# Optimization experiments

Hardware: AMD Instinct MI355X
Metric: run time of the kernel (lower is better)

The kernel has to match this reference:

```python
import jax, jax.numpy as jnp
import numpy as np

DIM = 256
HEADS = 8
WS = 8          # window_size[0]
N = WS * WS     # tokens per window
B = 2048        # number of windows (batch * windows_per_image)


def _rel_pos_indices(ws):
    # Reproduces: grid of (i,j) positions flattened, pairwise diff, shifted, flattened index
    pos = np.arange(ws)
    gy, gx = np.meshgrid(pos, pos, indexing='ij')
    grid = np.stack([gy.ravel(), gx.ravel()], axis=-1)          # (ws*ws, 2)
    rel = grid[:, None, :] - grid[None, :, :] + (ws - 1)        # (n, n, 2)
    idx = rel[..., 0] * (2 * ws - 1) + rel[..., 1]              # (n, n)
    return jnp.asarray(idx, dtype=jnp.int32)


def setup_inputs() -> dict:
    key = jax.random.key(0)
    ks = jax.random.split(key, 6)
    return {
        'x': jax.random.normal(ks[0], (B, N, DIM), dtype=jnp.float32),
        'qkv_w': jax.random.normal(ks[1], (3 * DIM, DIM), dtype=jnp.float32) * 0.02,
        'qkv_b': jax.random.normal(ks[2], (3 * DIM,), dtype=jnp.float32) * 0.02,
        'proj_w': jax.random.normal(ks[3], (DIM, DIM), dtype=jnp.float32) * 0.02,
        'proj_b': jax.random.normal(ks[4], (DIM,), dtype=jnp.float32) * 0.02,
        'bias_table': jax.random.normal(ks[5], ((2 * WS - 1) ** 2, HEADS), dtype=jnp.float32) * 0.02,
        'rel_pos_indices': _rel_pos_indices(WS),
    }


def reference(x, qkv_w, qkv_b, proj_w, proj_b, bias_table, rel_pos_indices):
    b, n, c = x.shape
    head_dim = c // HEADS
    scale = head_dim ** (-0.5)

    qkv = x @ qkv_w.T + qkv_b                                   # [b, n, 3c]
    q, k, v = jnp.split(qkv, 3, axis=-1)
    # b n (h d) -> b h n d
    to_heads = lambda t: t.reshape(b, n, HEADS, head_dim).transpose(0, 2, 1, 3)
    q, k, v = to_heads(q) * scale, to_heads(k), to_heads(v)

    # relative position bias: [n, n, h] -> [h, n, n]
    bias = bias_table[rel_pos_indices].transpose(2, 0, 1)

    attn = jnp.einsum('bhnd,bhmd->bhnm', q, k) + bias           # [b, h, n, n]
    attn = jax.nn.softmax(attn, axis=-1)
    out = jnp.einsum('bhnm,bhmd->bhnd', attn, v)                # [b, h, n, d]
    out = out.transpose(0, 2, 1, 3).reshape(b, n, c)
    out = out @ proj_w.T + proj_b
    return (out, attn)
```

## Files before the change

### kernel.cpp

```cpp
#include <hip/hip_runtime.h>

typedef __bf16 bf16;
typedef __attribute__((ext_vector_type(8))) __bf16 bf16x8;
typedef __attribute__((ext_vector_type(4))) __bf16 bf16x4;
typedef __attribute__((ext_vector_type(4))) float f32x4;

#define MFMA16(A, Bf, Cf) __builtin_amdgcn_mfma_f32_16x16x32_bf16((A), (Bf), (Cf), 0, 0, 0)

namespace {
constexpr int kB = 2048;
constexpr int kN = 64;
constexpr int kC = 256;
constexpr int kH = 8;
constexpr float kScale = 0.17677669529663687f;
constexpr size_t kOut0 = (size_t)kB * kN * kC;
constexpr size_t kWqkvOff = 0;
constexpr size_t kWprojOff = 393216;
constexpr size_t kBiasOff = 524288;
}

__global__ void prep_kernel(const float* __restrict__ qkv_w,
                            const float* __restrict__ proj_w,
                            const float* __restrict__ bias_table,
                            const int* __restrict__ rel_idx,
                            bf16* __restrict__ qkv_wb,
                            bf16* __restrict__ proj_wb,
                            float* __restrict__ biasf) {
  int t = blockIdx.x * 256 + threadIdx.x;
  if (t < 196608) {
    qkv_wb[t] = (bf16)qkv_w[t];
  } else if (t < 262144) {
    int u = t - 196608;
    proj_wb[u] = (bf16)proj_w[u];
  } else if (t < 294912) {
    int u = t - 262144;
    int h = u >> 12;
    int v = u & 4095;
    int wv = v >> 10;
    int ct = (v >> 8) & 3;
    int lane = (v >> 2) & 63;
    int r = v & 3;
    int row = wv * 16 + (lane >> 4) * 4 + r;
    int col = ct * 16 + (lane & 15);
    biasf[u] = bias_table[rel_idx[row * 64 + col] * 8 + h];
  }
}

__launch_bounds__(256, 3)
__global__ void attn_kernel(const float* __restrict__ x,
                            const float* __restrict__ qkv_b,
                            const float* __restrict__ proj_b,
                            const bf16* __restrict__ qkv_wb,
                            const bf16* __restrict__ proj_wb,
                            const float* __restrict__ biasf,
                            float* __restrict__ out,
                            float* __restrict__ attn_out) {
  __shared__ __align__(16) bf16 xo[64 * 264];
  __shared__ __align__(16) bf16 qp[64 * 72];
  __shared__ __align__(16) bf16 kh[64 * 40];
  __shared__ __align__(16) bf16 vT[32 * 72];

  const int t = threadIdx.x;
  const int wave = t >> 6;
  const int lane = t & 63;
  const int l16 = lane & 15;
  const int quad = lane >> 4;
  const int b = blockIdx.x;
  const int mrow = wave * 16 + l16;

  const f32x4 fzero = {0.f, 0.f, 0.f, 0.f};

  {
    const f32x4* xv = (const f32x4*)(x + (size_t)b * (kN * kC));
#pragma unroll
    for (int i = 0; i < 16; ++i) {
      int g4 = i * 256 + t;
      f32x4 v = xv[g4];
      int row = g4 >> 6;
      int c4 = (g4 & 63) << 2;
      bf16x4 w;
      w.x = (bf16)v.x; w.y = (bf16)v.y; w.z = (bf16)v.z; w.w = (bf16)v.w;
      *(bf16x4*)&xo[row * 264 + c4] = w;
    }
  }
  __syncthreads();

  bf16x8 afr[8];
#pragma unroll
  for (int kt = 0; kt < 8; ++kt)
    afr[kt] = *(const bf16x8*)&xo[mrow * 264 + kt * 32 + quad * 8];

  for (int h = 0; h < kH; ++h) {
    f32x4 bfrag[4];
    const f32x4* bp4 = (const f32x4*)(biasf + h * 4096 + wave * 1024);
#pragma unroll
    for (int ct = 0; ct < 4; ++ct) bfrag[ct] = bp4[ct * 64 + lane];
    float qbv[6];
#pragma unroll
    for (int nt = 0; nt < 6; ++nt) {
      int col = (nt & 1) * 16 + l16;
      qbv[nt] = qkv_b[((nt < 2) ? 0 : (nt < 4) ? 256 : 512) + h * 32 + col];
    }

    f32x4 acc[6];
#pragma unroll
    for (int nt = 0; nt < 6; ++nt) acc[nt] = fzero;
#pragma unroll
    for (int nt = 0; nt < 6; ++nt) {
      int wrow = (nt < 2) ? (h * 32 + nt * 16 + l16)
               : (nt < 4) ? (256 + h * 32 + (nt - 2) * 16 + l16)
                          : (512 + h * 32 + (nt - 4) * 16 + l16);
      const bf16* wp = qkv_wb + wrow * 256 + quad * 8;
      bf16x8 bfr[8];
#pragma unroll
      for (int kt = 0; kt < 8; ++kt) bfr[kt] = *(const bf16x8*)&wp[kt * 32];
#pragma unroll
      for (int kt = 0; kt < 8; ++kt) acc[nt] = MFMA16(afr[kt], bfr[kt], acc[nt]);
    }

    __syncthreads();

#pragma unroll
    for (int nt = 0; nt < 6; ++nt) {
      float qb = qbv[nt];
#pragma unroll
      for (int r = 0; r < 4; ++r) {
        int row = wave * 16 + quad * 4 + r;
        int col = (nt & 1) * 16 + l16;
        float val = acc[nt][r] + qb;
        if (nt < 2)       qp[row * 72 + col] = (bf16)(val * kScale);
        else if (nt < 4)  kh[row * 40 + col] = (bf16)val;
        else              vT[col * 72 + row] = (bf16)val;
      }
    }
    __syncthreads();

    bf16x8 aS = *(const bf16x8*)&qp[mrow * 72 + quad * 8];
    f32x4 s[4];
#pragma unroll
    for (int ct = 0; ct < 4; ++ct) {
      bf16x8 bS = *(const bf16x8*)&kh[(ct * 16 + l16) * 40 + quad * 8];
      s[ct] = MFMA16(aS, bS, bfrag[ct]);
    }

#pragma unroll
    for (int r = 0; r < 4; ++r) {
      float m = fmaxf(fmaxf(s[0][r], s[1][r]), fmaxf(s[2][r], s[3][r]));
#pragma unroll
      for (int off = 8; off; off >>= 1) m = fmaxf(m, __shfl_xor(m, off));
      float e0 = __expf(s[0][r] - m);
      float e1 = __expf(s[1][r] - m);
      float e2 = __expf(s[2][r] - m);
      float e3 = __expf(s[3][r] - m);
      float sum = (e0 + e1) + (e2 + e3);
#pragma unroll
      for (int off = 8; off; off >>= 1) sum += __shfl_xor(sum, off);
      float is = 1.0f / sum;
      s[0][r] = e0 * is; s[1][r] = e1 * is; s[2][r] = e2 * is; s[3][r] = e3 * is;
    }

    float* ao = attn_out + ((size_t)(b * kH + h) << 12);
#pragma unroll
    for (int ct = 0; ct < 4; ++ct)
#pragma unroll
      for (int r = 0; r < 4; ++r) {
        int i = wave * 16 + quad * 4 + r;
        int j = ct * 16 + l16;
        float pv = s[ct][r];
        ao[i * 64 + j] = pv;
        qp[i * 72 + j] = (bf16)pv;
      }

    f32x4 o[2];
    o[0] = fzero; o[1] = fzero;
#pragma unroll
    for (int ks = 0; ks < 2; ++ks) {
      bf16x8 aP = *(const bf16x8*)&qp[mrow * 72 + ks * 32 + quad * 8];
#pragma unroll
      for (int nt = 0; nt < 2; ++nt) {
        bf16x8 bV = *(const bf16x8*)&vT[(nt * 16 + l16) * 72 + ks * 32 + quad * 8];
        o[nt] = MFMA16(aP, bV, o[nt]);
      }
    }

#pragma unroll
    for (int nt = 0; nt < 2; ++nt)
#pragma unroll
      for (int r = 0; r < 4; ++r)
        xo[(wave * 16 + quad * 4 + r) * 264 + h * 32 + nt * 16 + l16] =
            (bf16)o[nt][r];
  }

  bf16x8 oafr[8];
#pragma unroll
  for (int kt = 0; kt < 8; ++kt)
    oafr[kt] = *(const bf16x8*)&xo[mrow * 264 + kt * 32 + quad * 8];

  f32x4 pacc[16];
#pragma unroll
  for (int i = 0; i < 16; ++i) pacc[i] = fzero;
#pragma unroll
  for (int nt = 0; nt < 16; ++nt) {
    const bf16* wp = proj_wb + (nt * 16 + l16) * 256 + quad * 8;
    bf16x8 bfr[8];
#pragma unroll
    for (int kt = 0; kt < 8; ++kt) bfr[kt] = *(const bf16x8*)&wp[kt * 32];
#pragma unroll
    for (int kt = 0; kt < 8; ++kt) pacc[nt] = MFMA16(oafr[kt], bfr[kt], pacc[nt]);
  }

  float* op = out + (size_t)b * (kN * kC);
#pragma unroll
  for (int nt = 0; nt < 16; ++nt) {
    float pb = proj_b[nt * 16 + l16];
#pragma unroll
    for (int r = 0; r < 4; ++r) {
      int i = wave * 16 + quad * 4 + r;
      op[i * 256 + nt * 16 + l16] = pacc[nt][r] + pb;
    }
  }
}

extern "C" void kernel_launch(void* const* d_in, const int* in_sizes, int n_in,
                              void* d_out, int out_size, void* d_ws, size_t ws_size,
                              hipStream_t stream) {
  const float* x          = (const float*)d_in[0];
  const float* qkv_w      = (const float*)d_in[1];
  const float* qkv_b      = (const float*)d_in[2];
  const float* proj_w     = (const float*)d_in[3];
  const float* proj_b     = (const float*)d_in[4];
  const float* bias_table = (const float*)d_in[5];
  const int*   rel_idx    = (const int*)d_in[6];

  bf16*  qkv_wb = (bf16*)((char*)d_ws + kWqkvOff);
  bf16*  proj_wb = (bf16*)((char*)d_ws + kWprojOff);
  float* biasf  = (float*)((char*)d_ws + kBiasOff);

  float* out      = (float*)d_out;
  float* attn_out = out + kOut0;

  prep_kernel<<<1152, 256, 0, stream>>>(qkv_w, proj_w, bias_table, rel_idx,
                                        qkv_wb, proj_wb, biasf);
  attn_kernel<<<kB, 256, 0, stream>>>(x, qkv_b, proj_b, qkv_wb, proj_wb, biasf,
                                      out, attn_out);
}
```

Measured before the change: 898.0 us.

## Split fused window attention into separate QKV, attention and projection kernels

Replaces the single fused kernel with three launches. The first computes the full QKV projection for a window using a 2x2 wave tiling, so each weight fragment is reused across two row tiles rather than reloaded by every wave for every head. Q/K and V are staged as bf16 in the not-yet-written regions of the output buffers, and a separate attention kernel and projection kernel read them back, with the next head's V transpose double-buffered in LDS. This trades redundant weight loads and per-head barriers for extra global round trips of intermediates and two more kernel launches.

New measurement: 929.5 us. +3.5%, slower.

```diff
diff --git a/kernel.cpp b/kernel.cpp
--- a/kernel.cpp
+++ b/kernel.cpp
@@ -9,15 +9,13 @@
 
 namespace {
 constexpr int kB = 2048;
-constexpr int kN = 64;
-constexpr int kC = 256;
-constexpr int kH = 8;
 constexpr float kScale = 0.17677669529663687f;
-constexpr size_t kOut0 = (size_t)kB * kN * kC;
+constexpr size_t kOut0 = (size_t)kB * 64 * 256;
 constexpr size_t kWqkvOff = 0;
 constexpr size_t kWprojOff = 393216;
 constexpr size_t kBiasOff = 524288;
 }
+
 
 __global__ void prep_kernel(const float* __restrict__ qkv_w,
                             const float* __restrict__ proj_w,
@@ -47,18 +45,85 @@
 }
 
 __launch_bounds__(256, 3)
-__global__ void attn_kernel(const float* __restrict__ x,
-                            const float* __restrict__ qkv_b,
-                            const float* __restrict__ proj_b,
-                            const bf16* __restrict__ qkv_wb,
-                            const bf16* __restrict__ proj_wb,
-                            const float* __restrict__ biasf,
-                            float* __restrict__ out,
-                            float* __restrict__ attn_out) {
-  __shared__ __align__(16) bf16 xo[64 * 264];
-  __shared__ __align__(16) bf16 qp[64 * 72];
-  __shared__ __align__(16) bf16 kh[64 * 40];
-  __shared__ __align__(16) bf16 vT[32 * 72];
+__global__ void qkv_kernel(const float* __restrict__ x,
+                           const float* __restrict__ qkv_b,
+                           const bf16* __restrict__ qkv_wb,
+                           float* __restrict__ out,
+                           float* __restrict__ attn_out) {
+  __shared__ __align__(16) bf16 xb[64 * 264];
+  const int t = threadIdx.x;
+  const int wave = t >> 6;
+  const int lane = t & 63;
+  const int l16 = lane & 15;
+  const int quad = lane >> 4;
+  const int b = blockIdx.x;
+  const int wr = wave >> 1;
+  const int wc = wave & 1;
+  const f32x4 fz = {0.f, 0.f, 0.f, 0.f};
+
+  {
+    const f32x4* xv = (const f32x4*)(x + (size_t)b * 16384);
+#pragma unroll
+    for (int i = 0; i < 16; ++i) {
+      int g4 = i * 256 + t;
+      f32x4 v = xv[g4];
+      int row = g4 >> 6;
+      int c4 = (g4 & 63) << 2;
+      bf16x4 w;
+      w.x = (bf16)v.x; w.y = (bf16)v.y; w.z = (bf16)v.z; w.w = (bf16)v.w;
+      *(bf16x4*)&xb[row * 264 + c4] = w;
+    }
+  }
+  __syncthreads();
+
+  bf16x8 afr[2][8];
+#pragma unroll
+  for (int rt = 0; rt < 2; ++rt)
+#pragma unroll
+    for (int kt = 0; kt < 8; ++kt)
+      afr[rt][kt] =
+          *(const bf16x8*)&xb[(wr * 32 + rt * 16 + l16) * 264 + kt * 32 + quad * 8];
+
+  bf16* qkst = (bf16*)(attn_out + (size_t)b * 32768);
+  bf16* vst  = (bf16*)(out + (size_t)b * 16384);
+
+#pragma unroll 2
+  for (int nt = 0; nt < 24; ++nt) {
+    int col16 = wc * 384 + nt * 16;
+    const bf16* wp = qkv_wb + (col16 + l16) * 256 + quad * 8;
+    bf16x8 bfr[8];
+#pragma unroll
+    for (int kt = 0; kt < 8; ++kt) bfr[kt] = *(const bf16x8*)&wp[kt * 32];
+    f32x4 a0 = fz, a1 = fz;
+#pragma unroll
+    for (int kt = 0; kt < 8; ++kt) {
+      a0 = MFMA16(afr[0][kt], bfr[kt], a0);
+      a1 = MFMA16(afr[1][kt], bfr[kt], a1);
+    }
+    int col = col16 + l16;
+    float qb = qkv_b[col];
+    float sc = (col16 < 256) ? kScale : 1.0f;
+#pragma unroll
+    for (int rt = 0; rt < 2; ++rt) {
+      f32x4 a = rt ? a1 : a0;
+#pragma unroll
+      for (int r = 0; r < 4; ++r) {
+        int row = wr * 32 + rt * 16 + quad * 4 + r;
+        float val = (a[r] + qb) * sc;
+        if (col16 < 512) qkst[row * 512 + col] = (bf16)val;
+        else             vst[row * 256 + (col - 512)] = (bf16)val;
+      }
+    }
+  }
+}
+
+__launch_bounds__(256, 3)
+__global__ void attn2_kernel(const float* __restrict__ biasf,
+                             float* __restrict__ out,
+                             float* __restrict__ attn_out) {
+  __shared__ __align__(16) bf16 kl[64 * 264];
+  __shared__ __align__(16) bf16 vT[2][32 * 72];
+  __shared__ __align__(16) bf16 Pb[64 * 72];
 
   const int t = threadIdx.x;
   const int wave = t >> 6;
@@ -67,80 +132,49 @@
   const int quad = lane >> 4;
   const int b = blockIdx.x;
   const int mrow = wave * 16 + l16;
-
-  const f32x4 fzero = {0.f, 0.f, 0.f, 0.f};
+  const f32x4 fz = {0.f, 0.f, 0.f, 0.f};
+
+  const bf16* qkst = (const bf16*)(attn_out + (size_t)b * 32768);
+  const bf16* vst  = (const bf16*)(out + (size_t)b * 16384);
+  bf16* ost = (bf16*)(out + (size_t)b * 16384) + 16384;
+
+  bf16x8 qf[8];
+#pragma unroll
+  for (int h = 0; h < 8; ++h)
+    qf[h] = *(const bf16x8*)&qkst[mrow * 512 + h * 32 + quad * 8];
 
   {
-    const f32x4* xv = (const f32x4*)(x + (size_t)b * (kN * kC));
-#pragma unroll
-    for (int i = 0; i < 16; ++i) {
-      int g4 = i * 256 + t;
-      f32x4 v = xv[g4];
-      int row = g4 >> 6;
-      int c4 = (g4 & 63) << 2;
-      bf16x4 w;
-      w.x = (bf16)v.x; w.y = (bf16)v.y; w.z = (bf16)v.z; w.w = (bf16)v.w;
-      *(bf16x4*)&xo[row * 264 + c4] = w;
-    }
+    int row = t >> 2, part = t & 3;
+#pragma unroll
+    for (int j = 0; j < 8; ++j) {
+      bf16x8 v = *(const bf16x8*)&qkst[row * 512 + 256 + part * 64 + j * 8];
+      *(bf16x8*)&kl[row * 264 + part * 64 + j * 8] = v;
+    }
+  }
+  {
+    int tok = t >> 2, dp = t & 3;
+    bf16x8 v = *(const bf16x8*)&vst[tok * 256 + dp * 8];
+#pragma unroll
+    for (int j = 0; j < 8; ++j) vT[0][(dp * 8 + j) * 72 + tok] = v[j];
   }
   __syncthreads();
 
-  bf16x8 afr[8];
-#pragma unroll
-  for (int kt = 0; kt < 8; ++kt)
-    afr[kt] = *(const bf16x8*)&xo[mrow * 264 + kt * 32 + quad * 8];
-
-  for (int h = 0; h < kH; ++h) {
+#pragma unroll
+  for (int h = 0; h < 8; ++h) {
+    int tok = t >> 2, dp = t & 3;
+    bf16x8 vnext;
+    if (h < 7) vnext = *(const bf16x8*)&vst[tok * 256 + (h + 1) * 32 + dp * 8];
+
     f32x4 bfrag[4];
     const f32x4* bp4 = (const f32x4*)(biasf + h * 4096 + wave * 1024);
 #pragma unroll
     for (int ct = 0; ct < 4; ++ct) bfrag[ct] = bp4[ct * 64 + lane];
-    float qbv[6];
-#pragma unroll
-    for (int nt = 0; nt < 6; ++nt) {
-      int col = (nt & 1) * 16 + l16;
-      qbv[nt] = qkv_b[((nt < 2) ? 0 : (nt < 4) ? 256 : 512) + h * 32 + col];
-    }
-
-    f32x4 acc[6];
-#pragma unroll
-    for (int nt = 0; nt < 6; ++nt) acc[nt] = fzero;
-#pragma unroll
-    for (int nt = 0; nt < 6; ++nt) {
-      int wrow = (nt < 2) ? (h * 32 + nt * 16 + l16)
-               : (nt < 4) ? (256 + h * 32 + (nt - 2) * 16 + l16)
-                          : (512 + h * 32 + (nt - 4) * 16 + l16);
-      const bf16* wp = qkv_wb + wrow * 256 + quad * 8;
-      bf16x8 bfr[8];
-#pragma unroll
-      for (int kt = 0; kt < 8; ++kt) bfr[kt] = *(const bf16x8*)&wp[kt * 32];
-#pragma unroll
-      for (int kt = 0; kt < 8; ++kt) acc[nt] = MFMA16(afr[kt], bfr[kt], acc[nt]);
-    }
-
-    __syncthreads();
-
-#pragma unroll
-    for (int nt = 0; nt < 6; ++nt) {
-      float qb = qbv[nt];
-#pragma unroll
-      for (int r = 0; r < 4; ++r) {
-        int row = wave * 16 + quad * 4 + r;
-        int col = (nt & 1) * 16 + l16;
-        float val = acc[nt][r] + qb;
-        if (nt < 2)       qp[row * 72 + col] = (bf16)(val * kScale);
-        else if (nt < 4)  kh[row * 40 + col] = (bf16)val;
-        else              vT[col * 72 + row] = (bf16)val;
-      }
-    }
-    __syncthreads();
-
-    bf16x8 aS = *(const bf16x8*)&qp[mrow * 72 + quad * 8];
+
     f32x4 s[4];
 #pragma unroll
     for (int ct = 0; ct < 4; ++ct) {
-      bf16x8 bS = *(const bf16x8*)&kh[(ct * 16 + l16) * 40 + quad * 8];
-      s[ct] = MFMA16(aS, bS, bfrag[ct]);
+      bf16x8 bS = *(const bf16x8*)&kl[(ct * 16 + l16) * 264 + h * 32 + quad * 8];
+      s[ct] = MFMA16(qf[h], bS, bfrag[ct]);
     }
 
 #pragma unroll
@@ -159,7 +193,7 @@
       s[0][r] = e0 * is; s[1][r] = e1 * is; s[2][r] = e2 * is; s[3][r] = e3 * is;
     }
 
-    float* ao = attn_out + ((size_t)(b * kH + h) << 12);
+    float* ao = attn_out + ((size_t)(b * 8 + h) << 12);
 #pragma unroll
     for (int ct = 0; ct < 4; ++ct)
 #pragma unroll
@@ -168,17 +202,17 @@
         int j = ct * 16 + l16;
         float pv = s[ct][r];
         ao[i * 64 + j] = pv;
-        qp[i * 72 + j] = (bf16)pv;
+        Pb[i * 72 + j] = (bf16)pv;
       }
 
     f32x4 o[2];
-    o[0] = fzero; o[1] = fzero;
+    o[0] = fz; o[1] = fz;
 #pragma unroll
     for (int ks = 0; ks < 2; ++ks) {
-      bf16x8 aP = *(const bf16x8*)&qp[mrow * 72 + ks * 32 + quad * 8];
+      bf16x8 aP = *(const bf16x8*)&Pb[mrow * 72 + ks * 32 + quad * 8];
 #pragma unroll
       for (int nt = 0; nt < 2; ++nt) {
-        bf16x8 bV = *(const bf16x8*)&vT[(nt * 16 + l16) * 72 + ks * 32 + quad * 8];
+        bf16x8 bV = *(const bf16x8*)&vT[h & 1][(nt * 16 + l16) * 72 + ks * 32 + quad * 8];
         o[nt] = MFMA16(aP, bV, o[nt]);
       }
     }
@@ -187,18 +221,40 @@
     for (int nt = 0; nt < 2; ++nt)
 #pragma unroll
       for (int r = 0; r < 4; ++r)
-        xo[(wave * 16 + quad * 4 + r) * 264 + h * 32 + nt * 16 + l16] =
+        ost[(wave * 16 + quad * 4 + r) * 256 + h * 32 + nt * 16 + l16] =
             (bf16)o[nt][r];
-  }
-
+
+    if (h < 7) {
+#pragma unroll
+      for (int j = 0; j < 8; ++j)
+        vT[(h + 1) & 1][(dp * 8 + j) * 72 + tok] = vnext[j];
+    }
+    __syncthreads();
+  }
+}
+
+__launch_bounds__(256, 3)
+__global__ void proj_kernel(const float* __restrict__ proj_b,
+                            const bf16* __restrict__ proj_wb,
+                            float* __restrict__ out) {
+  const int t = threadIdx.x;
+  const int wave = t >> 6;
+  const int lane = t & 63;
+  const int l16 = lane & 15;
+  const int quad = lane >> 4;
+  const int b = blockIdx.x;
+  const int mrow = wave * 16 + l16;
+  const f32x4 fz = {0.f, 0.f, 0.f, 0.f};
+
+  const bf16* ost = (const bf16*)(out + (size_t)b * 16384) + 16384;
   bf16x8 oafr[8];
 #pragma unroll
   for (int kt = 0; kt < 8; ++kt)
-    oafr[kt] = *(const bf16x8*)&xo[mrow * 264 + kt * 32 + quad * 8];
-
-  f32x4 pacc[16];
-#pragma unroll
-  for (int i = 0; i < 16; ++i) pacc[i] = fzero;
+    oafr[kt] = *(const bf16x8*)&ost[mrow * 256 + kt * 32 + quad * 8];
+
+  f32x4 acc[16];
+#pragma unroll
+  for (int i = 0; i < 16; ++i) acc[i] = fz;
 #pragma unroll
   for (int nt = 0; nt < 16; ++nt) {
     const bf16* wp = proj_wb + (nt * 16 + l16) * 256 + quad * 8;
@@ -206,18 +262,17 @@
 #pragma unroll
     for (int kt = 0; kt < 8; ++kt) bfr[kt] = *(const bf16x8*)&wp[kt * 32];
 #pragma unroll
-    for (int kt = 0; kt < 8; ++kt) pacc[nt] = MFMA16(oafr[kt], bfr[kt], pacc[nt]);
-  }
-
-  float* op = out + (size_t)b * (kN * kC);
+    for (int kt = 0; kt < 8; ++kt) acc[nt] = MFMA16(oafr[kt], bfr[kt], acc[nt]);
+  }
+  __syncthreads();
+
+  float* op = out + (size_t)b * 16384;
 #pragma unroll
   for (int nt = 0; nt < 16; ++nt) {
     float pb = proj_b[nt * 16 + l16];
 #pragma unroll
-    for (int r = 0; r < 4; ++r) {
-      int i = wave * 16 + quad * 4 + r;
-      op[i * 256 + nt * 16 + l16] = pacc[nt][r] + pb;
-    }
+    for (int r = 0; r < 4; ++r)
+      op[(wave * 16 + quad * 4 + r) * 256 + nt * 16 + l16] = acc[nt][r] + pb;
   }
 }
 
@@ -241,6 +296,7 @@
 
   prep_kernel<<<1152, 256, 0, stream>>>(qkv_w, proj_w, bias_table, rel_idx,
                                         qkv_wb, proj_wb, biasf);
-  attn_kernel<<<kB, 256, 0, stream>>>(x, qkv_b, proj_b, qkv_wb, proj_wb, biasf,
-                                      out, attn_out);
-}
+  qkv_kernel<<<kB, 256, 0, stream>>>(x, qkv_b, qkv_wb, out, attn_out);
+  attn2_kernel<<<kB, 256, 0, stream>>>(biasf, out, attn_out);
+  proj_kernel<<<kB, 256, 0, stream>>>(proj_b, proj_wb, out);
+}
```
